# Kernel optimization log

Measured on AMD Instinct MI355X. Metric: run time of the kernel, lower is better.

The kernel has to match this reference:

```python
import jax, jax.numpy as jnp
import numpy as np

NUM_BINS = 256


def _per_channel_hist(img):
    # img: [B, C, H, W] with histc range [0, 1].
    B, C, H, W = img.shape
    x = jnp.transpose(img, (1, 0, 2, 3)).reshape(C, -1)  # [C, N]
    # torch.histc: bin = floor(x * bins); value == max goes to last bin;
    # values outside [min, max] are ignored.
    idx = jnp.clip(jnp.floor(x * NUM_BINS).astype(jnp.int32), 0, NUM_BINS - 1)
    valid = ((x >= 0.0) & (x <= 1.0)).astype(img.dtype)  # [C, N]
    offsets = (jnp.arange(C, dtype=jnp.int32) * NUM_BINS)[:, None]
    flat_idx = (idx + offsets).reshape(-1)
    hist = jax.ops.segment_sum(valid.reshape(-1), flat_idx,
                               num_segments=C * NUM_BINS)
    return hist.reshape(C, NUM_BINS)


def setup_inputs() -> dict:
    key = jax.random.key(0)
    k1, k2 = jax.random.split(key)
    img1 = jax.random.uniform(k1, (16, 3, 512, 512), dtype=jnp.float32)
    img2 = jax.random.uniform(k2, (16, 3, 512, 512), dtype=jnp.float32)
    return {"img1": img1, "img2": img2}


def reference(img1, img2):
    h1 = _per_channel_hist(img1)  # [C, bins]
    h2 = _per_channel_hist(img2)
    h1 = h1 / jnp.sum(h1, axis=1, keepdims=True)
    h2 = h2 / jnp.sum(h2, axis=1, keepdims=True)
    cdf1 = jnp.cumsum(h1, axis=1)
    cdf2 = jnp.cumsum(h2, axis=1)
    loss = jnp.sum(jnp.abs(cdf1 - cdf2))  # sum over channels and bins
    return loss / 3.0
```

## Files before the change

### kernel.cpp

```cpp
#include <hip/hip_runtime.h>

#define NUM_BINS 256
#define HW4 65536
#define PLANES 16
#define GROUP_F4 (PLANES * HW4)
#define BLOCKS_PER_GROUP 256
#define THREADS 256
#define NCOPY 4

__global__ __launch_bounds__(THREADS) void hist_kernel(
    const float* __restrict__ img1,
    const float* __restrict__ img2,
    unsigned int* __restrict__ hist ) {

    __shared__ unsigned int lh[NCOPY][NUM_BINS];
    const int t = threadIdx.x;
    #pragma unroll
    for (int i = t; i < NCOPY * NUM_BINS; i += THREADS)
        ((unsigned int*)lh)[i] = 0u;
    __syncthreads();

    const int gid = blockIdx.x;
    const int group = gid / BLOCKS_PER_GROUP;
    const int blk = gid - group * BLOCKS_PER_GROUP;
    const int im = group / 3;
    const int c = group - im * 3;
    const float4* __restrict__ src =
        (const float4*)(im == 0 ? img1 : img2);
    unsigned int* lhw = lh[t >> 6];

    for (int k = blk * THREADS + t; k < GROUP_F4;
         k += BLOCKS_PER_GROUP * THREADS) {
        const int b = k >> 16;
        const int j = k & (HW4 - 1);
        const float4 v = src[(b * 3 + c) * HW4 + j];
        const float xs[4] = {v.x, v.y, v.z, v.w};
        #pragma unroll
        for (int e = 0; e < 4; ++e) {
            const float x = xs[e];
            if (x >= 0.0f && x <= 1.0f) {
                int bi = (int)(x * 256.0f);
                bi = bi > (NUM_BINS - 1) ? (NUM_BINS - 1) : bi;
                atomicAdd(&lhw[bi], 1u);
            }
        }
    }
    __syncthreads();

    const unsigned int s = lh[0][t] + lh[1][t] + lh[2][t] + lh[3][t];
    if (s) atomicAdd(&hist[group * NUM_BINS + t], s);
}

__global__ __launch_bounds__(NUM_BINS) void finalize_kernel(
    const unsigned int* __restrict__ hist, float* __restrict__ out) {

    __shared__ float b1[NUM_BINS];
    __shared__ float b2[NUM_BINS];
    __shared__ float red[NUM_BINS / 64];

    const int t = threadIdx.x;
    float acc = 0.0f;

    for (int c = 0; c < 3; ++c) {
        const float f1 = (float)hist[c * NUM_BINS + t];
        const float f2 = (float)hist[(3 + c) * NUM_BINS + t];
        b1[t] = f1;
        b2[t] = f2;
        __syncthreads();
        for (int off = 1; off < NUM_BINS; off <<= 1) {
            float a1 = 0.0f, a2 = 0.0f;
            if (t >= off) { a1 = b1[t - off]; a2 = b2[t - off]; }
            __syncthreads();
            b1[t] += a1;
            b2[t] += a2;
            __syncthreads();
        }
        const float s1 = b1[NUM_BINS - 1];
        const float s2 = b2[NUM_BINS - 1];
        acc += fabsf(b1[t] / s1 - b2[t] / s2);
        __syncthreads();
    }

    #pragma unroll
    for (int off = 32; off > 0; off >>= 1)
        acc += __shfl_down(acc, off, 64);
    if ((t & 63) == 0) red[t >> 6] = acc;
    __syncthreads();
    if (t == 0)
        out[0] = (red[0] + red[1] + red[2] + red[3]) * (1.0f / 3.0f);
}

extern "C" void kernel_launch(void* const* d_in, const int* in_sizes, int n_in,
                              void* d_out, int out_size, void* d_ws,
                              size_t ws_size, hipStream_t stream) {
    const float* img1 = (const float*)d_in[0];
    const float* img2 = (const float*)d_in[1];
    float* out = (float*)d_out;
    unsigned int* hist = (unsigned int*)d_ws;

    hipMemsetAsync(hist, 0, 6 * NUM_BINS * sizeof(unsigned int), stream);

    hist_kernel<<<6 * BLOCKS_PER_GROUP, THREADS, 0, stream>>>(img1, img2, hist);
    finalize_kernel<<<1, NUM_BINS, 0, stream>>>(hist, out);
}
```

Measured before the change: 122.2 us.

## Fuse finalize into histogram kernel via last-block counter and simplify addressing

After: 168.5 us. 1.38x slower.

```diff
diff --git a/kernel.cpp b/kernel.cpp
--- a/kernel.cpp
+++ b/kernel.cpp
@@ -3,37 +3,38 @@
 #define NUM_BINS 256
 #define HW4 65536
 #define PLANES 16
-#define GROUP_F4 (PLANES * HW4)
 #define BLOCKS_PER_GROUP 256
+#define NGROUPS 6
+#define GRID (NGROUPS * BLOCKS_PER_GROUP)
 #define THREADS 256
-#define NCOPY 4
 
-__global__ __launch_bounds__(THREADS) void hist_kernel(
+__global__ __launch_bounds__(THREADS) void hist_fused_kernel(
     const float* __restrict__ img1,
     const float* __restrict__ img2,
-    unsigned int* __restrict__ hist ) {
+    unsigned int* __restrict__ hist ,
+    unsigned int* __restrict__ counter,
+    float* __restrict__ out) {
 
-    __shared__ unsigned int lh[NCOPY][NUM_BINS];
+    __shared__ unsigned int lh[4][NUM_BINS];
+    __shared__ float red[THREADS / 64];
+    __shared__ int isLast;
+
     const int t = threadIdx.x;
-    #pragma unroll
-    for (int i = t; i < NCOPY * NUM_BINS; i += THREADS)
-        ((unsigned int*)lh)[i] = 0u;
+    lh[0][t] = 0u; lh[1][t] = 0u; lh[2][t] = 0u; lh[3][t] = 0u;
     __syncthreads();
 
     const int gid = blockIdx.x;
-    const int group = gid / BLOCKS_PER_GROUP;
-    const int blk = gid - group * BLOCKS_PER_GROUP;
-    const int im = group / 3;
+    const int group = gid >> 8;
+    const int blk = gid & (BLOCKS_PER_GROUP - 1);
+    const int im = (group >= 3) ? 1 : 0;
     const int c = group - im * 3;
     const float4* __restrict__ src =
-        (const float4*)(im == 0 ? img1 : img2);
+        (const float4*)(im ? img2 : img1) + (size_t)c * HW4 + blk * THREADS + t;
     unsigned int* lhw = lh[t >> 6];
 
-    for (int k = blk * THREADS + t; k < GROUP_F4;
-         k += BLOCKS_PER_GROUP * THREADS) {
-        const int b = k >> 16;
-        const int j = k & (HW4 - 1);
-        const float4 v = src[(b * 3 + c) * HW4 + j];
+    #pragma unroll 4
+    for (int it = 0; it < PLANES; ++it) {
+        const float4 v = src[(size_t)it * (3 * HW4)];
         const float xs[4] = {v.x, v.y, v.z, v.w};
         #pragma unroll
         for (int e = 0; e < 4; ++e) {
@@ -49,21 +50,24 @@
 
     const unsigned int s = lh[0][t] + lh[1][t] + lh[2][t] + lh[3][t];
     if (s) atomicAdd(&hist[group * NUM_BINS + t], s);
-}
+    __syncthreads();
 
-__global__ __launch_bounds__(NUM_BINS) void finalize_kernel(
-    const unsigned int* __restrict__ hist, float* __restrict__ out) {
+    if (t == 0) {
+        __threadfence();
+        const unsigned int prev = atomicAdd(counter, 1u);
+        isLast = (prev == (unsigned int)(GRID - 1));
+    }
+    __syncthreads();
+    if (!isLast) return;
+    __threadfence();
 
-    __shared__ float b1[NUM_BINS];
-    __shared__ float b2[NUM_BINS];
-    __shared__ float red[NUM_BINS / 64];
-
-    const int t = threadIdx.x;
+    float* b1 = (float*)lh[0];
+    float* b2 = (float*)lh[1];
     float acc = 0.0f;
 
-    for (int c = 0; c < 3; ++c) {
-        const float f1 = (float)hist[c * NUM_BINS + t];
-        const float f2 = (float)hist[(3 + c) * NUM_BINS + t];
+    for (int ch = 0; ch < 3; ++ch) {
+        const float f1 = (float)atomicAdd(&hist[ch * NUM_BINS + t], 0u);
+        const float f2 = (float)atomicAdd(&hist[(3 + ch) * NUM_BINS + t], 0u);
         b1[t] = f1;
         b2[t] = f2;
         __syncthreads();
@@ -75,9 +79,7 @@
             b2[t] += a2;
             __syncthreads();
         }
-        const float s1 = b1[NUM_BINS - 1];
-        const float s2 = b2[NUM_BINS - 1];
-        acc += fabsf(b1[t] / s1 - b2[t] / s2);
+        acc += fabsf(b1[t] / b1[NUM_BINS - 1] - b2[t] / b2[NUM_BINS - 1]);
         __syncthreads();
     }
 
@@ -97,9 +99,10 @@
     const float* img2 = (const float*)d_in[1];
     float* out = (float*)d_out;
     unsigned int* hist = (unsigned int*)d_ws;
+    unsigned int* counter = hist + NGROUPS * NUM_BINS;
 
-    hipMemsetAsync(hist, 0, 6 * NUM_BINS * sizeof(unsigned int), stream);
-
-    hist_kernel<<<6 * BLOCKS_PER_GROUP, THREADS, 0, stream>>>(img1, img2, hist);
-    finalize_kernel<<<1, NUM_BINS, 0, stream>>>(hist, out);
+    hipMemsetAsync(d_ws, 0, (NGROUPS * NUM_BINS + 1) * sizeof(unsigned int),
+                   stream);
+    hist_fused_kernel<<<GRID, THREADS, 0, stream>>>(img1, img2, hist, counter,
+                                                    out);
 }
```

## Use per-lane 16-bit shared histograms with single-wave blocks instead of LDS atomics

Applied to the files above, without the earlier changes.

Measured after the change: 193.4 us. 58.2% more time.

```diff
diff --git a/kernel.cpp b/kernel.cpp
--- a/kernel.cpp
+++ b/kernel.cpp
@@ -2,38 +2,40 @@
 
 #define NUM_BINS 256
 #define HW4 65536
-#define PLANES 16
-#define GROUP_F4 (PLANES * HW4)
+#define NGROUPS 6
 #define BLOCKS_PER_GROUP 256
-#define THREADS 256
-#define NCOPY 4
+#define THREADS 64
+#define F4_PER_BLOCK 4096
+#define ITERS (F4_PER_BLOCK / THREADS)
 
 __global__ __launch_bounds__(THREADS) void hist_kernel(
     const float* __restrict__ img1,
     const float* __restrict__ img2,
-    unsigned int* __restrict__ hist ) {
+    unsigned int* __restrict__ ghist ) {
 
-    __shared__ unsigned int lh[NCOPY][NUM_BINS];
-    const int t = threadIdx.x;
+    __shared__ unsigned short h16[NUM_BINS * 64];
+
+    const int lane = threadIdx.x;
+
+    uint4* z = (uint4*)h16;
     #pragma unroll
-    for (int i = t; i < NCOPY * NUM_BINS; i += THREADS)
-        ((unsigned int*)lh)[i] = 0u;
+    for (int i = 0; i < 32; ++i)
+        z[i * THREADS + lane] = make_uint4(0u, 0u, 0u, 0u);
     __syncthreads();
 
     const int gid = blockIdx.x;
-    const int group = gid / BLOCKS_PER_GROUP;
-    const int blk = gid - group * BLOCKS_PER_GROUP;
-    const int im = group / 3;
+    const int group = gid >> 8;
+    const int blk = gid & (BLOCKS_PER_GROUP - 1);
+    const int im = (group >= 3) ? 1 : 0;
     const int c = group - im * 3;
+    const int b = blk >> 4;
+    const int joff = (blk & 15) * F4_PER_BLOCK;
     const float4* __restrict__ src =
-        (const float4*)(im == 0 ? img1 : img2);
-    unsigned int* lhw = lh[t >> 6];
+        (const float4*)(im ? img2 : img1) + (size_t)(b * 3 + c) * HW4 + joff + lane;
 
-    for (int k = blk * THREADS + t; k < GROUP_F4;
-         k += BLOCKS_PER_GROUP * THREADS) {
-        const int b = k >> 16;
-        const int j = k & (HW4 - 1);
-        const float4 v = src[(b * 3 + c) * HW4 + j];
+    #pragma unroll 4
+    for (int it = 0; it < ITERS; ++it) {
+        const float4 v = src[it * THREADS];
         const float xs[4] = {v.x, v.y, v.z, v.w};
         #pragma unroll
         for (int e = 0; e < 4; ++e) {
@@ -41,14 +43,26 @@
             if (x >= 0.0f && x <= 1.0f) {
                 int bi = (int)(x * 256.0f);
                 bi = bi > (NUM_BINS - 1) ? (NUM_BINS - 1) : bi;
-                atomicAdd(&lhw[bi], 1u);
+                const int idx = (bi << 6) | lane;
+                h16[idx] = (unsigned short)(h16[idx] + 1u);
             }
         }
     }
     __syncthreads();
 
-    const unsigned int s = lh[0][t] + lh[1][t] + lh[2][t] + lh[3][t];
-    if (s) atomicAdd(&hist[group * NUM_BINS + t], s);
+    #pragma unroll
+    for (int q = 0; q < 4; ++q) {
+        const int bin = (q << 6) | lane;
+        const uint4* row = (const uint4*)&h16[bin << 6];
+        unsigned int s = 0;
+        #pragma unroll
+        for (int cc = 0; cc < 8; ++cc) {
+            const uint4 w = row[(cc + lane) & 7];
+            s += (w.x & 0xffffu) + (w.x >> 16) + (w.y & 0xffffu) + (w.y >> 16)
+               + (w.z & 0xffffu) + (w.z >> 16) + (w.w & 0xffffu) + (w.w >> 16);
+        }
+        if (s) atomicAdd(&ghist[group * NUM_BINS + bin], s);
+    }
 }
 
 __global__ __launch_bounds__(NUM_BINS) void finalize_kernel(
@@ -62,10 +76,8 @@
     float acc = 0.0f;
 
     for (int c = 0; c < 3; ++c) {
-        const float f1 = (float)hist[c * NUM_BINS + t];
-        const float f2 = (float)hist[(3 + c) * NUM_BINS + t];
-        b1[t] = f1;
-        b2[t] = f2;
+        b1[t] = (float)hist[c * NUM_BINS + t];
+        b2[t] = (float)hist[(3 + c) * NUM_BINS + t];
         __syncthreads();
         for (int off = 1; off < NUM_BINS; off <<= 1) {
             float a1 = 0.0f, a2 = 0.0f;
@@ -75,9 +87,7 @@
             b2[t] += a2;
             __syncthreads();
         }
-        const float s1 = b1[NUM_BINS - 1];
-        const float s2 = b2[NUM_BINS - 1];
-        acc += fabsf(b1[t] / s1 - b2[t] / s2);
+        acc += fabsf(b1[t] / b1[NUM_BINS - 1] - b2[t] / b2[NUM_BINS - 1]);
         __syncthreads();
     }
 
@@ -98,8 +108,9 @@
     float* out = (float*)d_out;
     unsigned int* hist = (unsigned int*)d_ws;
 
-    hipMemsetAsync(hist, 0, 6 * NUM_BINS * sizeof(unsigned int), stream);
+    hipMemsetAsync(hist, 0, NGROUPS * NUM_BINS * sizeof(unsigned int), stream);
 
-    hist_kernel<<<6 * BLOCKS_PER_GROUP, THREADS, 0, stream>>>(img1, img2, hist);
+    hist_kernel<<<NGROUPS * BLOCKS_PER_GROUP, THREADS, 0, stream>>>(img1, img2,
+                                                                    hist);
     finalize_kernel<<<1, NUM_BINS, 0, stream>>>(hist, out);
 }
```
